# Optimization experiments

Hardware: AMD Instinct MI355X
Metric: run time of the kernel (lower is better)

Reference implementation:

```python
import jax, jax.numpy as jnp
import numpy as np

K = 8  # search_range in sample_wise_recolor
BIG = 1e30


def setup_inputs() -> dict:
    key = jax.random.key(0)
    ks = jax.random.split(key, 6)
    L, N = 16384, 10000  # L: upsampled candidate voxels (multiple of 8), N: target points
    pred_F = jax.random.normal(ks[0], (L,), jnp.float32)
    cand_xyz = jax.random.normal(ks[1], (L, 3), jnp.float32) * 50.0
    cand_rgb = jax.random.uniform(ks[2], (L, 3), jnp.float32)
    tgt_xyz = jax.random.normal(ks[3], (N, 3), jnp.float32) * 50.0
    tgt_rgb = jax.random.uniform(ks[4], (N, 3), jnp.float32)
    keep_target = jax.random.randint(ks[5], (L,), 0, 2, jnp.int32)
    return {"pred_F": pred_F, "cand_xyz": cand_xyz, "cand_rgb": cand_rgb,
            "tgt_xyz": tgt_xyz, "tgt_rgb": tgt_rgb, "keep_target": keep_target,
            "points_num": 8192}


def _get_keep(pred, points_num):
    # local-max mask over groups of 8 children (scatter of per-row argmax)
    L = pred.shape[0]
    p8 = pred.reshape(-1, 8)
    rows = jnp.arange(p8.shape[0])
    is_local_max = jnp.zeros(p8.shape, dtype=bool).at[rows, jnp.argmax(p8, axis=1)].set(True).reshape(-1)
    # kthvalue over the non-local-max subset: local-max entries pushed to +inf so the
    # k-th smallest of the full sorted array equals the k-th smallest of the subset.
    k = L - points_num  # static python int
    vals = jnp.where(is_local_max, jnp.inf, pred)
    threshold = jnp.sort(vals)[k - 1]
    return (pred > threshold) | is_local_max


def _pairwise_sqdist(a, b):
    # a: [P,3], b: [Q,3] -> [P,Q] squared distances
    a2 = jnp.sum(a * a, axis=1)
    b2 = jnp.sum(b * b, axis=1)
    d2 = a2[:, None] + b2[None, :] - 2.0 * (a @ b.T)
    return jnp.maximum(d2, 0.0)


def _recolor_loss(cand_xyz, rgb, keep, tgt_xyz, tgt_rgb):
    L = cand_xyz.shape[0]
    N = tgt_xyz.shape[0]
    d2 = _pairwise_sqdist(tgt_xyz, cand_xyz)  # [N, L]

    # ---- recolor_backward: KNN from each target point into kept candidates ----
    d_masked = jnp.where(keep[None, :], d2, BIG)
    neg_d, idx = jax.lax.top_k(-d_masked, K)  # [N, K]
    d = -neg_d
    zero_mask = d == 0.0
    min_mask = (d == jnp.min(d, axis=1, keepdims=True)) & ~jnp.any(zero_mask, axis=1)[:, None]
    w = jnp.where(min_mask, 1.0 / jnp.sqrt(jnp.maximum(d, 1e-30)), 0.0)  # [N, K]

    flat_idx = idx.reshape(-1)
    num = jnp.zeros((L, 3), rgb.dtype).at[flat_idx].add((tgt_rgb[:, None, :] * w[:, :, None]).reshape(-1, 3))
    den = jnp.zeros((L,), rgb.dtype).at[flat_idx].add(w.reshape(-1))
    has_den = den != 0.0
    recolored = jnp.where(has_den[:, None], num / jnp.where(has_den, den, 1.0)[:, None], 0.0)

    # exact-match (zero-distance) targets overwrite; scatter with safe out-of-range dummy row
    safe_idx = jnp.where(zero_mask, idx, L).reshape(-1)
    tgt_exp = jnp.broadcast_to(tgt_rgb[:, None, :], (N, K, 3)).reshape(-1, 3)
    recolored = jnp.concatenate([recolored, jnp.zeros((1, 3), rgb.dtype)], 0).at[safe_idx].set(tgt_exp)[:L]
    empty = jnp.concatenate([~has_den, jnp.zeros((1,), bool)], 0).at[safe_idx].set(False)[:L]
    empty = empty & keep  # only kept candidates matter

    # ---- recolor_forward: kept candidates with no color yet pull from nearest targets ----
    neg_df, idxf = jax.lax.top_k(-d2.T, K)  # [L, K]
    df = -neg_df
    mf = df == jnp.min(df, axis=1, keepdims=True)
    rec_fwd = jnp.sum(tgt_rgb[idxf] * mf[:, :, None], axis=1) / jnp.sum(mf, axis=1, keepdims=True).astype(rgb.dtype)
    recolored = jnp.where(empty[:, None], rec_fwd, recolored)

    # L1 loss over kept candidates only; recolor target is no-grad in the original
    recolored = jax.lax.stop_gradient(recolored)
    return jnp.sum(jnp.where(keep[:, None], jnp.abs(rgb - recolored), 0.0))


def reference(pred_F, cand_xyz, cand_rgb, tgt_xyz, tgt_rgb, keep_target, points_num):
    keep = _get_keep(jax.lax.stop_gradient(pred_F), points_num)  # @torch.no_grad
    # coord recon loss: BCE-with-logits, reduction='sum'
    t = keep_target.astype(pred_F.dtype)
    coord_loss = jnp.sum(jnp.maximum(pred_F, 0.0) - pred_F * t + jnp.log1p(jnp.exp(-jnp.abs(pred_F))))
    # inverse_transform_for_color in training mode: x * 255
    rgb = cand_rgb * 255.0
    rgb_loss = _recolor_loss(cand_xyz, rgb, keep, tgt_xyz, tgt_rgb)
    return jnp.stack([coord_loss, rgb_loss])
```

## Files before the change

### kernel.cpp

```cpp
#include <hip/hip_runtime.h>
#include <hip/hip_bf16.h>


#define SCAN_T 256
#define CHUNK  128
typedef unsigned long long ull;

__device__ __forceinline__ void select_bin(
    unsigned int* hist, int nb, unsigned int rank,
    unsigned int* sB, unsigned int* sR, int tid) {
  if (tid < 64) {
    int g = nb >> 6;
    unsigned int sum = 0;
    for (int j = 0; j < g; ++j) sum += hist[tid * g + j];
    unsigned int incl = sum;
    for (int o = 1; o < 64; o <<= 1) {
      unsigned int v = __shfl_up(incl, o);
      if (tid >= o) incl += v;
    }
    unsigned int excl = incl - sum;
    bool cond = (rank >= excl) && (rank < incl);
    unsigned long long bal = __ballot(cond);
    int first = __ffsll((long long)bal) - 1;
    if (tid == first) {
      unsigned int r = rank - excl, cum = 0;
      for (int j = 0; j < g; ++j) {
        unsigned int c = hist[tid * g + j];
        if (r < cum + c) { *sB = (unsigned int)(tid * g + j); *sR = r - cum; break; }
        cum += c;
      }
    }
  }
}

__global__ __launch_bounds__(1024) void k_init_sel(
    const float* __restrict__ pred, const float* __restrict__ txyz,
    const float* __restrict__ cxyz, const int* __restrict__ ktgt,
    const int* __restrict__ pnum_p,
    float4* __restrict__ ttile, float4* __restrict__ numden,
    int* __restrict__ zerohit, ull* __restrict__ tmin, ull* __restrict__ fmin,
    unsigned char* __restrict__ islm, int* __restrict__ keep,
    float4* __restrict__ klist, int* __restrict__ kidx,
    int* counters, float* __restrict__ out, float* __restrict__ thr_out,
    int L, int N, int IB) {
  __shared__ unsigned int skey[16384];
  __shared__ unsigned int hist[2048];
  __shared__ unsigned int sB, sR;
  __shared__ float s_thr;
  int tid = threadIdx.x;

  if ((int)blockIdx.x < IB) {
    int gidx = blockIdx.x * 1024 + tid;
    int gsz = IB * 1024;
    for (int i = gidx; i < N; i += gsz) {
      float x = txyz[3*i], y = txyz[3*i+1], z = txyz[3*i+2];
      ttile[i] = make_float4(x, y, z, fmaf(x, x, fmaf(y, y, z * z)));
      tmin[i] = ~0ull;
    }
    for (int i = gidx; i < L; i += gsz) {
      numden[i] = make_float4(0.f, 0.f, 0.f, 0.f);
      zerohit[i] = 0;
      fmin[i] = ~0ull;
    }
    if (tid == 0) {
      while (__hip_atomic_load(&counters[15], __ATOMIC_ACQUIRE,
                               __HIP_MEMORY_SCOPE_AGENT) == 0)
        __builtin_amdgcn_s_sleep(8);
      s_thr = thr_out[0];
    }
    __syncthreads();
    float thr = s_thr;
    float term = 0.f;
    for (int i = gidx; i < L; i += gsz) {
      float p = pred[i];
      bool kp = (p > thr) || islm[i];
      keep[i] = kp ? 1 : 0;
      if (kp) {
        int pos = atomicAdd(&counters[0], 1);
        float x = cxyz[3*i], y = cxyz[3*i+1], z = cxyz[3*i+2];
        klist[pos] = make_float4(x, y, z, fmaf(x, x, fmaf(y, y, z * z)));
        kidx[pos] = i;
      }
      float t = (float)ktgt[i];
      term += fmaxf(p, 0.f) - p * t + log1pf(expf(-fabsf(p)));
    }
    for (int o = 32; o > 0; o >>= 1) term += __shfl_down(term, o);
    if ((tid & 63) == 0) atomicAdd(&out[0], term);
    return;
  }

  int ngroups = L >> 3;
  for (int g = tid; g < ngroups; g += 1024) {
    const float4* pv = (const float4*)pred + (size_t)g * 2;
    float4 a = pv[0], b = pv[1];
    float v[8] = {a.x, a.y, a.z, a.w, b.x, b.y, b.z, b.w};
    int bi = 0; float bv = v[0];
    #pragma unroll
    for (int j = 1; j < 8; ++j) if (v[j] > bv) { bv = v[j]; bi = j; }
    ull lmpack = 0ull;
    #pragma unroll
    for (int j = 0; j < 8; ++j) {
      unsigned int fb = __float_as_uint(v[j]);
      unsigned int mk = (fb & 0x80000000u) ? ~fb : (fb | 0x80000000u);
      if (j == bi) { mk = 0xFF800000u; lmpack |= 1ull << (8 * j); }
      skey[g * 8 + j] = mk;
    }
    *(ull*)(islm + (size_t)g * 8) = lmpack;
  }
  __syncthreads();

  unsigned int rank = (unsigned int)(L - pnum_p[0] - 1);
  const uint4* s4 = (const uint4*)skey;
  int n4 = L >> 2;
  for (int b = tid; b < 2048; b += 1024) hist[b] = 0u;
  __syncthreads();
  for (int i = tid; i < n4; i += 1024) {
    uint4 v = s4[i];
    atomicAdd(&hist[v.x >> 21], 1u); atomicAdd(&hist[v.y >> 21], 1u);
    atomicAdd(&hist[v.z >> 21], 1u); atomicAdd(&hist[v.w >> 21], 1u);
  }
  __syncthreads();
  select_bin(hist, 2048, rank, &sB, &sR, tid);
  __syncthreads();
  unsigned int B1 = sB, R1 = sR;
  for (int b = tid; b < 2048; b += 1024) hist[b] = 0u;
  __syncthreads();
  for (int i = tid; i < n4; i += 1024) {
    uint4 v = s4[i];
    if ((v.x >> 21) == B1) atomicAdd(&hist[(v.x >> 10) & 2047u], 1u);
    if ((v.y >> 21) == B1) atomicAdd(&hist[(v.y >> 10) & 2047u], 1u);
    if ((v.z >> 21) == B1) atomicAdd(&hist[(v.z >> 10) & 2047u], 1u);
    if ((v.w >> 21) == B1) atomicAdd(&hist[(v.w >> 10) & 2047u], 1u);
  }
  __syncthreads();
  select_bin(hist, 2048, R1, &sB, &sR, tid);
  __syncthreads();
  unsigned int B2 = sB, R2 = sR;
  for (int b = tid; b < 1024; b += 1024) hist[b] = 0u;
  __syncthreads();
  unsigned int top22 = (B1 << 11) | B2;
  for (int i = tid; i < n4; i += 1024) {
    uint4 v = s4[i];
    if ((v.x >> 10) == top22) atomicAdd(&hist[v.x & 1023u], 1u);
    if ((v.y >> 10) == top22) atomicAdd(&hist[v.y & 1023u], 1u);
    if ((v.z >> 10) == top22) atomicAdd(&hist[v.z & 1023u], 1u);
    if ((v.w >> 10) == top22) atomicAdd(&hist[v.w & 1023u], 1u);
  }
  __syncthreads();
  select_bin(hist, 1024, R2, &sB, &sR, tid);
  __syncthreads();
  if (tid == 0) {
    unsigned int fkey = (B1 << 21) | (B2 << 10) | sB;
    unsigned int fb = (fkey & 0x80000000u) ? (fkey & 0x7FFFFFFFu) : ~fkey;
    thr_out[0] = __uint_as_float(fb);
    out[0] = 0.f; out[1] = 0.f;
    #pragma unroll
    for (int c = 0; c < 8; ++c) counters[c] = 0;
  }
  __syncthreads();
  if (tid == 0)
    __hip_atomic_store(&counters[15], 1, __ATOMIC_RELEASE,
                       __HIP_MEMORY_SCOPE_AGENT);
}

__global__ __launch_bounds__(SCAN_T) void k_scan2(
    const float* __restrict__ txyz, const float4* __restrict__ klist,
    const int* __restrict__ kidx, const float4* __restrict__ ttile,
    const int* __restrict__ counters, ull* __restrict__ tmin,
    ull* __restrict__ fmin, int L, int N, int YB) {
  __shared__ float4 tile[CHUNK];
  int tid = threadIdx.x, x = blockIdx.x, y = blockIdx.y;
  int kc = counters[0];

  if (y < YB) {
    int c0 = y * CHUNK;
    if (x * 1024 >= N || c0 >= kc) return;
    int cnt = min(CHUNK, kc - c0);
    if (tid < cnt) tile[tid] = klist[c0 + tid];
    __syncthreads();
    int tb = x * 1024 + tid;
    float ntx[4], nty[4], ntz[4], best[4];
    int bpos[4];
    bool act[4];
    #pragma unroll
    for (int j = 0; j < 4; ++j) {
      int t = tb + 256 * j;
      act[j] = t < N;
      float tx = 0.f, ty = 0.f, tz = 0.f;
      if (act[j]) { tx = txyz[3*t]; ty = txyz[3*t+1]; tz = txyz[3*t+2]; }
      ntx[j] = -2.f * tx; nty[j] = -2.f * ty; ntz[j] = -2.f * tz;
      best[j] = 3e38f; bpos[j] = 0;
    }
    #pragma unroll 4
    for (int c = 0; c < cnt; ++c) {
      float4 cd = tile[c];
      #pragma unroll
      for (int j = 0; j < 4; ++j) {
        float d = fmaf(ntx[j], cd.x, cd.w);
        d = fmaf(nty[j], cd.y, d);
        d = fmaf(ntz[j], cd.z, d);
        if (d < best[j]) { best[j] = d; bpos[j] = c; }
      }
    }
    #pragma unroll
    for (int j = 0; j < 4; ++j) {
      if (act[j]) {
        int p = c0 + bpos[j];
        float4 cd = klist[p];
        float tx = -0.5f * ntx[j], ty = -0.5f * nty[j], tz = -0.5f * ntz[j];
        float dx = tx - cd.x, dy = ty - cd.y, dz = tz - cd.z;
        float dtrue = fmaf(dx, dx, fmaf(dy, dy, dz * dz));
        ull pack = ((ull)__float_as_uint(dtrue) << 32) | (unsigned int)kidx[p];
        atomicMin(&tmin[tb + 256 * j], pack);
      }
    }
  } else {
    int t0 = (y - YB) * CHUNK;
    if (x * 1024 >= kc || t0 >= N) return;
    int tcnt = min(CHUNK, N - t0);
    if (tid < tcnt) tile[tid] = ttile[t0 + tid];
    __syncthreads();
    int eb = x * 1024 + tid;
    float ncx[4], ncy[4], ncz[4], c2[4], best[4];
    int bpos[4], li[4];
    bool act[4];
    #pragma unroll
    for (int j = 0; j < 4; ++j) {
      int e = eb + 256 * j;
      act[j] = e < kc;
      float cx = 0.f, cy = 0.f, cz = 0.f;
      c2[j] = 0.f; li[j] = 0;
      if (act[j]) {
        float4 cd = klist[e];
        cx = cd.x; cy = cd.y; cz = cd.z; c2[j] = cd.w;
        li[j] = kidx[e];
      }
      ncx[j] = -2.f * cx; ncy[j] = -2.f * cy; ncz[j] = -2.f * cz;
      best[j] = 3e38f; bpos[j] = 0;
    }
    #pragma unroll 4
    for (int c = 0; c < tcnt; ++c) {
      float4 td = tile[c];
      #pragma unroll
      for (int j = 0; j < 4; ++j) {
        float d = fmaf(ncx[j], td.x, td.w);
        d = fmaf(ncy[j], td.y, d);
        d = fmaf(ncz[j], td.z, d);
        if (d < best[j]) { best[j] = d; bpos[j] = c; }
      }
    }
    #pragma unroll
    for (int j = 0; j < 4; ++j) {
      if (act[j]) {
        float dkey = fmaxf(best[j] + c2[j], 0.f);
        ull pack = ((ull)__float_as_uint(dkey) << 32) |
                   (unsigned int)(t0 + bpos[j]);
        atomicMin(&fmin[li[j]], pack);
      }
    }
  }
}

__global__ __launch_bounds__(256) void k_scatter(
    const float* __restrict__ trgb, const ull* __restrict__ tmin,
    float4* __restrict__ numden, int* __restrict__ zerohit,
    float4* __restrict__ zcolor, int N) {
  int t = blockIdx.x * 256 + threadIdx.x;
  if (t >= N) return;
  ull pack = tmin[t];
  float d = __uint_as_float((unsigned int)(pack >> 32));
  int idx = (int)(pack & 0xFFFFFFFFull);
  float r = trgb[3*t], g = trgb[3*t+1], b = trgb[3*t+2];
  if (d == 0.0f) {
    zerohit[idx] = 1;
    zcolor[idx] = make_float4(r, g, b, 0.f);
  } else {
    float w = 1.0f / sqrtf(fmaxf(d, 1e-30f));
    atomicAdd(&numden[idx].x, r * w);
    atomicAdd(&numden[idx].y, g * w);
    atomicAdd(&numden[idx].z, b * w);
    atomicAdd(&numden[idx].w, w);
  }
}

__global__ __launch_bounds__(256) void k_loss(
    const float* __restrict__ crgb, const float* __restrict__ trgb,
    const int* __restrict__ keep, const float4* __restrict__ numden,
    const int* __restrict__ zerohit, const float4* __restrict__ zcolor,
    const ull* __restrict__ fmin, float* __restrict__ out, int L) {
  int l = blockIdx.x * 256 + threadIdx.x;
  float loss = 0.f;
  if (l < L && keep[l]) {
    float rr, rg, rb;
    if (zerohit[l]) {
      float4 z = zcolor[l]; rr = z.x; rg = z.y; rb = z.z;
    } else {
      float4 nd = numden[l];
      if (nd.w != 0.f) { rr = nd.x / nd.w; rg = nd.y / nd.w; rb = nd.z / nd.w; }
      else {
        int ti = (int)(fmin[l] & 0xFFFFFFFFull);
        rr = trgb[3*ti]; rg = trgb[3*ti+1]; rb = trgb[3*ti+2];
      }
    }
    float sr = crgb[3*l]*255.f, sg = crgb[3*l+1]*255.f, sb = crgb[3*l+2]*255.f;
    loss = fabsf(sr - rr) + fabsf(sg - rg) + fabsf(sb - rb);
  }
  for (int o = 32; o > 0; o >>= 1) loss += __shfl_down(loss, o);
  if ((threadIdx.x & 63) == 0) atomicAdd(&out[1], loss);
}

extern "C" void kernel_launch(void* const* d_in, const int* in_sizes, int n_in,
                              void* d_out, int out_size, void* d_ws, size_t ws_size,
                              hipStream_t stream) {
  const float* pred = (const float*)d_in[0];
  const float* cxyz = (const float*)d_in[1];
  const float* crgb = (const float*)d_in[2];
  const float* txyz = (const float*)d_in[3];
  const float* trgb = (const float*)d_in[4];
  const int*   ktgt = (const int*)d_in[5];
  const int*   pnum = (const int*)d_in[6];
  int L = in_sizes[0];
  int N = in_sizes[3] / 3;

  char* ws = (char*)d_ws;
  size_t off = 0;
  float4* klist  = (float4*)(ws + off);   off += (size_t)L * 16;
  float4* ttile  = (float4*)(ws + off);   off += (size_t)((N + 3) & ~3) * 16;
  float4* numden = (float4*)(ws + off);   off += (size_t)L * 16;
  float4* zcolor = (float4*)(ws + off);   off += (size_t)L * 16;
  ull* tmin      = (ull*)(ws + off);      off += (size_t)((N + 1) & ~1) * 8;
  ull* fmin      = (ull*)(ws + off);      off += (size_t)L * 8;
  int* keep      = (int*)(ws + off);      off += (size_t)L * 4;
  int* kidx      = (int*)(ws + off);      off += (size_t)L * 4;
  int* zerohit   = (int*)(ws + off);      off += (size_t)L * 4;
  float* thr_slot = (float*)(ws + off);   off += 16;
  int* counters  = (int*)(ws + off);      off += 256;
  unsigned char* islm = (unsigned char*)(ws + off); off += ((size_t)L + 15) & ~15ull;
  float* out = (float*)d_out;

  int nbL = (L + 255) / 256;
  int nbN = (N + 255) / 256;
  int mx = max(L, N);

  hipMemsetAsync((void*)(counters + 15), 0, 4, stream);

  int IB = (mx + 1023) / 1024;
  k_init_sel<<<IB + 1, 1024, 0, stream>>>(
      pred, txyz, cxyz, ktgt, pnum, ttile, numden, zerohit, tmin, fmin,
      islm, keep, klist, kidx, counters, out, thr_slot, L, N, IB);

  int gx = (mx + 1023) / 1024;
  int YB = (L + CHUNK - 1) / CHUNK;
  int YF = (N + CHUNK - 1) / CHUNK;
  dim3 gs(gx, YB + YF);
  k_scan2<<<gs, SCAN_T, 0, stream>>>(
      txyz, klist, kidx, ttile, counters, tmin, fmin, L, N, YB);

  k_scatter<<<nbN, 256, 0, stream>>>(trgb, tmin, numden, zerohit, zcolor, N);

  k_loss<<<nbL, 256, 0, stream>>>(
      crgb, trgb, keep, numden, zerohit, zcolor, fmin, out, L);
}
```

Baseline: 132.6 us.

## Run forward nearest-target scan only for kept candidates left without color

The fused scan kernel is split into a backward scan and a forward scan. A new compaction kernel runs after the scatter and lists the kept candidates that received no weight and no exact hit. The forward scan then searches targets only for that compacted list, not for every kept candidate. This removes most of the forward brute-force distance work, at the cost of two extra launches and the loss of overlap between the backward and forward scans. It relies on counters[1] being zeroed by the init kernel, which it is.

```diff
diff --git a/kernel.cpp b/kernel.cpp
--- a/kernel.cpp
+++ b/kernel.cpp
@@ -163,100 +163,52 @@
                        __HIP_MEMORY_SCOPE_AGENT);
 }
 
-__global__ __launch_bounds__(SCAN_T) void k_scan2(
+__global__ __launch_bounds__(SCAN_T) void k_scan_bwd(
     const float* __restrict__ txyz, const float4* __restrict__ klist,
-    const int* __restrict__ kidx, const float4* __restrict__ ttile,
-    const int* __restrict__ counters, ull* __restrict__ tmin,
-    ull* __restrict__ fmin, int L, int N, int YB) {
+    const int* __restrict__ kidx, const int* __restrict__ counters,
+    ull* __restrict__ tmin, int N) {
   __shared__ float4 tile[CHUNK];
   int tid = threadIdx.x, x = blockIdx.x, y = blockIdx.y;
   int kc = counters[0];
-
-  if (y < YB) {
-    int c0 = y * CHUNK;
-    if (x * 1024 >= N || c0 >= kc) return;
-    int cnt = min(CHUNK, kc - c0);
-    if (tid < cnt) tile[tid] = klist[c0 + tid];
-    __syncthreads();
-    int tb = x * 1024 + tid;
-    float ntx[4], nty[4], ntz[4], best[4];
-    int bpos[4];
-    bool act[4];
+  int c0 = y * CHUNK;
+  if (x * 1024 >= N || c0 >= kc) return;
+  int cnt = min(CHUNK, kc - c0);
+  if (tid < cnt) tile[tid] = klist[c0 + tid];
+  __syncthreads();
+  int tb = x * 1024 + tid;
+  float ntx[4], nty[4], ntz[4], best[4];
+  int bpos[4];
+  bool act[4];
+  #pragma unroll
+  for (int j = 0; j < 4; ++j) {
+    int t = tb + 256 * j;
+    act[j] = t < N;
+    float tx = 0.f, ty = 0.f, tz = 0.f;
+    if (act[j]) { tx = txyz[3*t]; ty = txyz[3*t+1]; tz = txyz[3*t+2]; }
+    ntx[j] = -2.f * tx; nty[j] = -2.f * ty; ntz[j] = -2.f * tz;
+    best[j] = 3e38f; bpos[j] = 0;
+  }
+  #pragma unroll 4
+  for (int c = 0; c < cnt; ++c) {
+    float4 cd = tile[c];
     #pragma unroll
     for (int j = 0; j < 4; ++j) {
-      int t = tb + 256 * j;
-      act[j] = t < N;
-      float tx = 0.f, ty = 0.f, tz = 0.f;
-      if (act[j]) { tx = txyz[3*t]; ty = txyz[3*t+1]; tz = txyz[3*t+2]; }
-      ntx[j] = -2.f * tx; nty[j] = -2.f * ty; ntz[j] = -2.f * tz;
-      best[j] = 3e38f; bpos[j] = 0;
-    }
-    #pragma unroll 4
-    for (int c = 0; c < cnt; ++c) {
-      float4 cd = tile[c];
-      #pragma unroll
-      for (int j = 0; j < 4; ++j) {
-        float d = fmaf(ntx[j], cd.x, cd.w);
-        d = fmaf(nty[j], cd.y, d);
-        d = fmaf(ntz[j], cd.z, d);
-        if (d < best[j]) { best[j] = d; bpos[j] = c; }
-      }
-    }
-    #pragma unroll
-    for (int j = 0; j < 4; ++j) {
-      if (act[j]) {
-        int p = c0 + bpos[j];
-        float4 cd = klist[p];
-        float tx = -0.5f * ntx[j], ty = -0.5f * nty[j], tz = -0.5f * ntz[j];
-        float dx = tx - cd.x, dy = ty - cd.y, dz = tz - cd.z;
-        float dtrue = fmaf(dx, dx, fmaf(dy, dy, dz * dz));
-        ull pack = ((ull)__float_as_uint(dtrue) << 32) | (unsigned int)kidx[p];
-        atomicMin(&tmin[tb + 256 * j], pack);
-      }
-    }
-  } else {
-    int t0 = (y - YB) * CHUNK;
-    if (x * 1024 >= kc || t0 >= N) return;
-    int tcnt = min(CHUNK, N - t0);
-    if (tid < tcnt) tile[tid] = ttile[t0 + tid];
-    __syncthreads();
-    int eb = x * 1024 + tid;
-    float ncx[4], ncy[4], ncz[4], c2[4], best[4];
-    int bpos[4], li[4];
-    bool act[4];
-    #pragma unroll
-    for (int j = 0; j < 4; ++j) {
-      int e = eb + 256 * j;
-      act[j] = e < kc;
-      float cx = 0.f, cy = 0.f, cz = 0.f;
-      c2[j] = 0.f; li[j] = 0;
-      if (act[j]) {
-        float4 cd = klist[e];
-        cx = cd.x; cy = cd.y; cz = cd.z; c2[j] = cd.w;
-        li[j] = kidx[e];
-      }
-      ncx[j] = -2.f * cx; ncy[j] = -2.f * cy; ncz[j] = -2.f * cz;
-      best[j] = 3e38f; bpos[j] = 0;
-    }
-    #pragma unroll 4
-    for (int c = 0; c < tcnt; ++c) {
-      float4 td = tile[c];
-      #pragma unroll
-      for (int j = 0; j < 4; ++j) {
-        float d = fmaf(ncx[j], td.x, td.w);
-        d = fmaf(ncy[j], td.y, d);
-        d = fmaf(ncz[j], td.z, d);
-        if (d < best[j]) { best[j] = d; bpos[j] = c; }
-      }
-    }
-    #pragma unroll
-    for (int j = 0; j < 4; ++j) {
-      if (act[j]) {
-        float dkey = fmaxf(best[j] + c2[j], 0.f);
-        ull pack = ((ull)__float_as_uint(dkey) << 32) |
-                   (unsigned int)(t0 + bpos[j]);
-        atomicMin(&fmin[li[j]], pack);
-      }
+      float d = fmaf(ntx[j], cd.x, cd.w);
+      d = fmaf(nty[j], cd.y, d);
+      d = fmaf(ntz[j], cd.z, d);
+      if (d < best[j]) { best[j] = d; bpos[j] = c; }
+    }
+  }
+  #pragma unroll
+  for (int j = 0; j < 4; ++j) {
+    if (act[j]) {
+      int p = c0 + bpos[j];
+      float4 cd = klist[p];
+      float tx = -0.5f * ntx[j], ty = -0.5f * nty[j], tz = -0.5f * ntz[j];
+      float dx = tx - cd.x, dy = ty - cd.y, dz = tz - cd.z;
+      float dtrue = fmaf(dx, dx, fmaf(dy, dy, dz * dz));
+      ull pack = ((ull)__float_as_uint(dtrue) << 32) | (unsigned int)kidx[p];
+      atomicMin(&tmin[tb + 256 * j], pack);
     }
   }
 }
@@ -283,6 +235,73 @@
   }
 }
 
+__global__ __launch_bounds__(256) void k_empty(
+    const float4* __restrict__ klist, const int* __restrict__ kidx,
+    const float4* __restrict__ numden, const int* __restrict__ zerohit,
+    int* counters, float4* __restrict__ elist, int* __restrict__ eidx) {
+  int e = blockIdx.x * 256 + threadIdx.x;
+  int kc = counters[0];
+  if (e >= kc) return;
+  int l = kidx[e];
+  if (numden[l].w == 0.f && !zerohit[l]) {
+    int pos = atomicAdd(&counters[1], 1);
+    elist[pos] = klist[e];
+    eidx[pos] = l;
+  }
+}
+
+__global__ __launch_bounds__(SCAN_T) void k_scan_fwd(
+    const float4* __restrict__ elist, const int* __restrict__ eidx,
+    const float4* __restrict__ ttile, const int* __restrict__ counters,
+    ull* __restrict__ fmin, int N) {
+  __shared__ float4 tile[CHUNK];
+  int tid = threadIdx.x, x = blockIdx.x, y = blockIdx.y;
+  int ec = counters[1];
+  int t0 = y * CHUNK;
+  if (x * 1024 >= ec || t0 >= N) return;
+  int tcnt = min(CHUNK, N - t0);
+  if (tid < tcnt) tile[tid] = ttile[t0 + tid];
+  __syncthreads();
+  int eb = x * 1024 + tid;
+  float ncx[4], ncy[4], ncz[4], c2[4], best[4];
+  int bpos[4], li[4];
+  bool act[4];
+  #pragma unroll
+  for (int j = 0; j < 4; ++j) {
+    int e = eb + 256 * j;
+    act[j] = e < ec;
+    float cx = 0.f, cy = 0.f, cz = 0.f;
+    c2[j] = 0.f; li[j] = 0;
+    if (act[j]) {
+      float4 cd = elist[e];
+      cx = cd.x; cy = cd.y; cz = cd.z; c2[j] = cd.w;
+      li[j] = eidx[e];
+    }
+    ncx[j] = -2.f * cx; ncy[j] = -2.f * cy; ncz[j] = -2.f * cz;
+    best[j] = 3e38f; bpos[j] = 0;
+  }
+  #pragma unroll 4
+  for (int c = 0; c < tcnt; ++c) {
+    float4 td = tile[c];
+    #pragma unroll
+    for (int j = 0; j < 4; ++j) {
+      float d = fmaf(ncx[j], td.x, td.w);
+      d = fmaf(ncy[j], td.y, d);
+      d = fmaf(ncz[j], td.z, d);
+      if (d < best[j]) { best[j] = d; bpos[j] = c; }
+    }
+  }
+  #pragma unroll
+  for (int j = 0; j < 4; ++j) {
+    if (act[j]) {
+      float dkey = fmaxf(best[j] + c2[j], 0.f);
+      ull pack = ((ull)__float_as_uint(dkey) << 32) |
+                 (unsigned int)(t0 + bpos[j]);
+      atomicMin(&fmin[li[j]], pack);
+    }
+  }
+}
+
 __global__ __launch_bounds__(256) void k_loss(
     const float* __restrict__ crgb, const float* __restrict__ trgb,
     const int* __restrict__ keep, const float4* __restrict__ numden,
@@ -328,11 +347,13 @@
   float4* ttile  = (float4*)(ws + off);   off += (size_t)((N + 3) & ~3) * 16;
   float4* numden = (float4*)(ws + off);   off += (size_t)L * 16;
   float4* zcolor = (float4*)(ws + off);   off += (size_t)L * 16;
+  float4* elist  = (float4*)(ws + off);   off += (size_t)L * 16;
   ull* tmin      = (ull*)(ws + off);      off += (size_t)((N + 1) & ~1) * 8;
   ull* fmin      = (ull*)(ws + off);      off += (size_t)L * 8;
   int* keep      = (int*)(ws + off);      off += (size_t)L * 4;
   int* kidx      = (int*)(ws + off);      off += (size_t)L * 4;
   int* zerohit   = (int*)(ws + off);      off += (size_t)L * 4;
+  int* eidx      = (int*)(ws + off);      off += (size_t)L * 4;
   float* thr_slot = (float*)(ws + off);   off += 16;
   int* counters  = (int*)(ws + off);      off += 256;
   unsigned char* islm = (unsigned char*)(ws + off); off += ((size_t)L + 15) & ~15ull;
@@ -349,14 +370,22 @@
       pred, txyz, cxyz, ktgt, pnum, ttile, numden, zerohit, tmin, fmin,
       islm, keep, klist, kidx, counters, out, thr_slot, L, N, IB);
 
-  int gx = (mx + 1023) / 1024;
-  int YB = (L + CHUNK - 1) / CHUNK;
-  int YF = (N + CHUNK - 1) / CHUNK;
-  dim3 gs(gx, YB + YF);
-  k_scan2<<<gs, SCAN_T, 0, stream>>>(
-      txyz, klist, kidx, ttile, counters, tmin, fmin, L, N, YB);
+  {
+    dim3 gb((N + 1023) / 1024, (L + CHUNK - 1) / CHUNK);
+    k_scan_bwd<<<gb, SCAN_T, 0, stream>>>(
+        txyz, klist, kidx, counters, tmin, N);
+  }
 
   k_scatter<<<nbN, 256, 0, stream>>>(trgb, tmin, numden, zerohit, zcolor, N);
+
+  k_empty<<<nbL, 256, 0, stream>>>(
+      klist, kidx, numden, zerohit, counters, elist, eidx);
+
+  {
+    dim3 gf((L + 1023) / 1024, (N + CHUNK - 1) / CHUNK);
+    k_scan_fwd<<<gf, SCAN_T, 0, stream>>>(
+        elist, eidx, ttile, counters, fmin, N);
+  }
 
   k_loss<<<nbL, 256, 0, stream>>>(
       crgb, trgb, keep, numden, zerohit, zcolor, fmin, out, L);
```

After: 139.4 us. +5.1%, slower.
